# Optimization experiments

Measured on AMD Instinct MI355X. Metric: run time of the kernel, lower is better.

## Reference

```python
import jax, jax.numpy as jnp
import numpy as np

B, T, V, E, HID = 32, 128, 32000, 256, 512


def setup_inputs() -> dict:
    key = jax.random.key(0)
    ks = jax.random.split(key, 5)
    s_e, s_h, s_i, s_u = 1.0 / np.sqrt(E), 1.0 / np.sqrt(HID), 1.0 / np.sqrt(E), 1.0 / np.sqrt(HID)
    return {
        "input_x": jax.random.randint(ks[0], (B, T), 0, V, dtype=jnp.int32),
        "initial_state": jnp.zeros((B, HID), dtype=jnp.float32),
        "embedding": jax.random.normal(ks[1], (V, E), dtype=jnp.float32) * s_e,
        "H": jax.random.normal(ks[2], (HID, HID), dtype=jnp.float32) * s_h,
        "I": jax.random.normal(ks[3], (E, HID), dtype=jnp.float32) * s_i,
        "b1": jnp.zeros((HID,), dtype=jnp.float32),
        "U": jax.random.normal(ks[4], (HID, V), dtype=jnp.float32) * s_u,
        "b2": jnp.zeros((V,), dtype=jnp.float32),
    }


def reference(input_x, initial_state, embedding, H, I, b1, U, b2):
    # Embedding lookup: [B, T, E] -> time-major [T, B, E]
    emb = embedding[input_x]                      # [B, T, E]
    xs = jnp.transpose(emb, (1, 0, 2))            # [T, B, E]
    # Dropout is identity in eval mode (p=0.0).

    def step(h, x_t):
        h_new = jax.nn.relu(h @ H + x_t @ I + b1)  # [B, HID]
        return h_new, h_new

    last_state, hs = jax.lax.scan(step, initial_state, xs)  # hs: [T, B, HID]
    # Vocab projection for all steps at once: [T, B, V]
    logits = jnp.einsum("tbh,hv->tbv", hs, U) + b2
    logits = jnp.transpose(logits, (1, 0, 2))     # [B, T, V]
    return logits, last_state
```

## Files before the change

kernel.cpp:

```cpp
#include <hip/hip_runtime.h>
#include <hip/hip_bf16.h>
#include <stdint.h>

#define B_ 32
#define T_ 128
#define V_ 32000
#define E_ 256
#define HID_ 512

typedef float f32x4 __attribute__((ext_vector_type(4)));
typedef __bf16 bf16x8 __attribute__((ext_vector_type(8)));

static __device__ __forceinline__ unsigned short f2bf(float f) {
    unsigned int u = __float_as_uint(f);
    unsigned int r = (u + 0x7fffu + ((u >> 16) & 1u)) >> 16;
    return (unsigned short)r;
}

__global__ __launch_bounds__(512) void k_embed_proj(
    const int* __restrict__ x, const float* __restrict__ emb,
    const float* __restrict__ I, const float* __restrict__ b1,
    float* __restrict__ C) {
    __shared__ float e[16][E_];
    const int tid = threadIdx.x;
    const int row0 = blockIdx.x * 16;

#pragma unroll
    for (int p = 0; p < 2; ++p) {
        int flat = p * 2048 + tid * 4;
        int i = flat >> 8;
        int c = flat & 255;
        int r = row0 + i;
        int t = r >> 5, b = r & 31;
        int xi = x[b * T_ + t];
        *(f32x4*)&e[i][c] = *(const f32x4*)(emb + (size_t)xi * E_ + c);
    }
    __syncthreads();

    float acc[16];
#pragma unroll
    for (int i = 0; i < 16; ++i) acc[i] = 0.f;
    const int j = tid;

    for (int k4 = 0; k4 < E_ / 4; ++k4) {
        float Iv[4];
#pragma unroll
        for (int q = 0; q < 4; ++q) Iv[q] = I[(size_t)(k4 * 4 + q) * HID_ + j];
#pragma unroll
        for (int i = 0; i < 16; ++i) {
            f32x4 ev = *(const f32x4*)&e[i][k4 * 4];
            acc[i] += ev[0] * Iv[0];
            acc[i] += ev[1] * Iv[1];
            acc[i] += ev[2] * Iv[2];
            acc[i] += ev[3] * Iv[3];
        }
    }
    float bv = b1[j];
#pragma unroll
    for (int i = 0; i < 16; ++i)
        C[(size_t)(row0 + i) * HID_ + j] = acc[i] + bv;
}

__global__ __launch_bounds__(256) void k_hconv(const float* __restrict__ H,
                                               unsigned short* __restrict__ Hb) {
    int idx = (blockIdx.x * 256 + threadIdx.x) * 4;
    f32x4 v = *(const f32x4*)(H + idx);
    unsigned int p0 = (unsigned)f2bf(v[0]) | ((unsigned)f2bf(v[1]) << 16);
    unsigned int p1 = (unsigned)f2bf(v[2]) | ((unsigned)f2bf(v[3]) << 16);
    uint2 pp; pp.x = p0; pp.y = p1;
    *(uint2*)(Hb + idx) = pp;
}

__global__ __launch_bounds__(256) void k_transpose(const float* __restrict__ U,
                                                   unsigned short* __restrict__ Ut) {
    __shared__ float tile[64][65];
    const int tid = threadIdx.x;
    const int n0 = blockIdx.x * 64;
    const int k0 = blockIdx.y * 64;
    const int c = tid & 63;
    const int r = tid >> 6;
#pragma unroll
    for (int it = 0; it < 16; ++it) {
        int kk = it * 4 + r;
        tile[kk][c] = U[(size_t)(k0 + kk) * V_ + n0 + c];
    }
    __syncthreads();
#pragma unroll
    for (int it = 0; it < 16; ++it) {
        int nn = it * 4 + r;
        Ut[(size_t)(n0 + nn) * HID_ + k0 + c] = f2bf(tile[c][nn]);
    }
}

__global__ __launch_bounds__(512) void k_recur(
    const float* __restrict__ C, const unsigned short* __restrict__ Hb,
    const float* __restrict__ init, unsigned short* __restrict__ hsb,
    float* __restrict__ lastState) {
    __shared__ float h[HID_];
    __shared__ float ps[8][HID_];
    const int tid = threadIdx.x;
    const int b = blockIdx.x;
    const int kg = tid >> 6;
    const int cg = tid & 63;
    const int j0 = cg * 8;
    const int kbase = kg * 64;

    h[tid] = init[b * HID_ + tid];
    __syncthreads();

    for (int t = 0; t < T_; ++t) {
        float cv = C[((size_t)t * B_ + b) * HID_ + tid];
        float a0 = 0, a1 = 0, a2 = 0, a3 = 0, a4 = 0, a5 = 0, a6 = 0, a7 = 0;
#pragma unroll 4
        for (int k4 = 0; k4 < 16; ++k4) {
            f32x4 hv = *(const f32x4*)&h[kbase + k4 * 4];
#pragma unroll
            for (int q = 0; q < 4; ++q) {
                const uint4 u = *(const uint4*)(Hb + (size_t)(kbase + k4 * 4 + q) * HID_ + j0);
                float hq = hv[q];
                a0 += hq * __uint_as_float(u.x << 16);
                a1 += hq * __uint_as_float(u.x & 0xffff0000u);
                a2 += hq * __uint_as_float(u.y << 16);
                a3 += hq * __uint_as_float(u.y & 0xffff0000u);
                a4 += hq * __uint_as_float(u.z << 16);
                a5 += hq * __uint_as_float(u.z & 0xffff0000u);
                a6 += hq * __uint_as_float(u.w << 16);
                a7 += hq * __uint_as_float(u.w & 0xffff0000u);
            }
        }
        f32x4 w0 = {a0, a1, a2, a3};
        f32x4 w1 = {a4, a5, a6, a7};
        *(f32x4*)&ps[kg][j0] = w0;
        *(f32x4*)&ps[kg][j0 + 4] = w1;
        __syncthreads();

        float v = cv;
#pragma unroll
        for (int g = 0; g < 8; ++g) v += ps[g][tid];
        v = fmaxf(v, 0.f);
        h[tid] = v;
        hsb[((size_t)t * B_ + b) * HID_ + tid] = f2bf(v);
        __syncthreads();
    }
    lastState[b * HID_ + tid] = h[tid];
}

#define LDK 72
__global__ __launch_bounds__(256) void k_gemm(
    const unsigned short* __restrict__ A, const unsigned short* __restrict__ Bt,
    const float* __restrict__ b2, float* __restrict__ out) {
    __shared__ unsigned short As[128 * LDK];
    __shared__ unsigned short Bs[128 * LDK];
    const int tid = threadIdx.x;
    const int l = tid & 63;
    const int w = tid >> 6;
    const int wm = w >> 1, wn = w & 1;
    const int n0 = blockIdx.x * 128;
    const int m0 = blockIdx.y * 128;

    f32x4 acc[4][4] = {};

    for (int kt = 0; kt < 8; ++kt) {
        const int kk = kt * 64;
        uint4 ra[4], rb[4];
#pragma unroll
        for (int i = 0; i < 4; ++i) {
            int flat = i * 256 + tid;
            int row = flat >> 3;
            int c8 = (flat & 7) * 8;
            ra[i] = *(const uint4*)(A + (size_t)(m0 + row) * HID_ + kk + c8);
            rb[i] = *(const uint4*)(Bt + (size_t)(n0 + row) * HID_ + kk + c8);
        }
        __syncthreads();
#pragma unroll
        for (int i = 0; i < 4; ++i) {
            int flat = i * 256 + tid;
            int row = flat >> 3;
            int c8 = (flat & 7) * 8;
            *(uint4*)(As + row * LDK + c8) = ra[i];
            *(uint4*)(Bs + row * LDK + c8) = rb[i];
        }
        __syncthreads();
#pragma unroll
        for (int ks = 0; ks < 2; ++ks) {
            bf16x8 af[4], bfr[4];
#pragma unroll
            for (int f = 0; f < 4; ++f) {
                af[f]  = *(const bf16x8*)(As + (wm * 64 + f * 16 + (l & 15)) * LDK + ks * 32 + (l >> 4) * 8);
                bfr[f] = *(const bf16x8*)(Bs + (wn * 64 + f * 16 + (l & 15)) * LDK + ks * 32 + (l >> 4) * 8);
            }
#pragma unroll
            for (int fm = 0; fm < 4; ++fm)
#pragma unroll
                for (int fn = 0; fn < 4; ++fn)
                    acc[fm][fn] = __builtin_amdgcn_mfma_f32_16x16x32_bf16(
                        af[fm], bfr[fn], acc[fm][fn], 0, 0, 0);
        }
    }

    const int cl = l & 15;
    const int q4 = (l >> 4) * 4;
    float b2v[4];
#pragma unroll
    for (int fn = 0; fn < 4; ++fn) b2v[fn] = b2[n0 + wn * 64 + fn * 16 + cl];
#pragma unroll
    for (int fm = 0; fm < 4; ++fm) {
#pragma unroll
        for (int r = 0; r < 4; ++r) {
            int rg = m0 + wm * 64 + fm * 16 + q4 + r;
            int t = rg >> 5, b = rg & 31;
            float* orow = out + (size_t)(b * T_ + t) * V_ + n0 + wn * 64 + cl;
#pragma unroll
            for (int fn = 0; fn < 4; ++fn)
                orow[fn * 16] = acc[fm][fn][r] + b2v[fn];
        }
    }
}

extern "C" void kernel_launch(void* const* d_in, const int* in_sizes, int n_in,
                              void* d_out, int out_size, void* d_ws, size_t ws_size,
                              hipStream_t stream) {
    const int* x      = (const int*)d_in[0];
    const float* init = (const float*)d_in[1];
    const float* emb  = (const float*)d_in[2];
    const float* H    = (const float*)d_in[3];
    const float* I    = (const float*)d_in[4];
    const float* b1   = (const float*)d_in[5];
    const float* U    = (const float*)d_in[6];
    const float* b2   = (const float*)d_in[7];
    float* out = (float*)d_out;

    char* ws = (char*)d_ws;
    float* C            = (float*)ws;
    unsigned short* hsb = (unsigned short*)(ws + ((size_t)8 << 20));
    unsigned short* Ut  = (unsigned short*)(ws + ((size_t)12 << 20));
    unsigned short* Hb  = (unsigned short*)(ws + ((size_t)46 << 20));

    k_embed_proj<<<256, 512, 0, stream>>>(x, emb, I, b1, C);
    k_hconv<<<(HID_ * HID_) / (256 * 4), 256, 0, stream>>>(H, Hb);
    k_transpose<<<dim3(500, 8), 256, 0, stream>>>(U, Ut);
    k_recur<<<B_, 512, 0, stream>>>(C, Hb, init, hsb, out + (size_t)B_ * T_ * V_);
    k_gemm<<<dim3(250, 32), 256, 0, stream>>>(hsb, Ut, b2, out);
}
```

Measured before the change: 1.774 ms.

## Split recurrence across four blocks per batch with register-resident H slices

The recurrent kernel now uses four cooperating blocks per batch row, each holding a 128-row slice of the bf16 H matrix in registers instead of re-reading H from global memory every step. Partial sums are exchanged through a global scratch area (the output buffer, which the later GEMM overwrites) with per-step release/acquire flags, and the kernel is launched cooperatively with 128 blocks. This is meant to cut the per-step global-memory traffic for H and spread the serial recurrence over more CUs. In exchange it adds a cross-block flag handshake on every timestep, a memset, and pressure from 64 registers per thread for the H slice.

Measured after the change: 3.280 ms. 1.85x slower.

```diff
diff --git a/kernel.cpp b/kernel.cpp
--- a/kernel.cpp
+++ b/kernel.cpp
@@ -95,54 +95,88 @@
 __global__ __launch_bounds__(512) void k_recur(
     const float* __restrict__ C, const unsigned short* __restrict__ Hb,
     const float* __restrict__ init, unsigned short* __restrict__ hsb,
-    float* __restrict__ lastState) {
+    float* __restrict__ lastState, float* __restrict__ xbuf,
+    int* __restrict__ xflag) {
     __shared__ float h[HID_];
-    __shared__ float ps[8][HID_];
-    const int tid = threadIdx.x;
-    const int b = blockIdx.x;
-    const int kg = tid >> 6;
-    const int cg = tid & 63;
-    const int j0 = cg * 8;
-    const int kbase = kg * 64;
-
-    h[tid] = init[b * HID_ + tid];
+    __shared__ unsigned short stage[32][HID_];
+    const int tid = threadIdx.x;
+    const int b = blockIdx.x >> 2;
+    const int g = blockIdx.x & 3;
+    const int j = tid;
+
+    unsigned int Hreg[64];
+#pragma unroll
+    for (int c4 = 0; c4 < 4; ++c4) {
+#pragma unroll
+        for (int i = 0; i < 4; ++i) {
+            int idx = i * 512 + tid;
+            int rr = idx >> 6;
+            int col = (idx & 63) * 8;
+            *(uint4*)&stage[rr][col] =
+                *(const uint4*)(Hb + (size_t)(g * 128 + c4 * 32 + rr) * HID_ + col);
+        }
+        __syncthreads();
+#pragma unroll
+        for (int rr = 0; rr < 32; rr += 2) {
+            unsigned int lo = stage[rr][j];
+            unsigned int hi = stage[rr + 1][j];
+            Hreg[(c4 * 32 + rr) >> 1] = lo | (hi << 16);
+        }
+        __syncthreads();
+    }
+
+    if (tid < HID_) h[tid] = init[b * HID_ + tid];
     __syncthreads();
 
     for (int t = 0; t < T_; ++t) {
-        float cv = C[((size_t)t * B_ + b) * HID_ + tid];
-        float a0 = 0, a1 = 0, a2 = 0, a3 = 0, a4 = 0, a5 = 0, a6 = 0, a7 = 0;
-#pragma unroll 4
-        for (int k4 = 0; k4 < 16; ++k4) {
-            f32x4 hv = *(const f32x4*)&h[kbase + k4 * 4];
-#pragma unroll
-            for (int q = 0; q < 4; ++q) {
-                const uint4 u = *(const uint4*)(Hb + (size_t)(kbase + k4 * 4 + q) * HID_ + j0);
-                float hq = hv[q];
-                a0 += hq * __uint_as_float(u.x << 16);
-                a1 += hq * __uint_as_float(u.x & 0xffff0000u);
-                a2 += hq * __uint_as_float(u.y << 16);
-                a3 += hq * __uint_as_float(u.y & 0xffff0000u);
-                a4 += hq * __uint_as_float(u.z << 16);
-                a5 += hq * __uint_as_float(u.z & 0xffff0000u);
-                a6 += hq * __uint_as_float(u.w << 16);
-                a7 += hq * __uint_as_float(u.w & 0xffff0000u);
+        float cv = C[((size_t)t * B_ + b) * HID_ + j];
+        float acc = 0.f;
+#pragma unroll
+        for (int kb = 0; kb < 8; ++kb) {
+            f32x4 hv[4];
+#pragma unroll
+            for (int q = 0; q < 4; ++q)
+                hv[q] = *(const f32x4*)&h[g * 128 + kb * 16 + q * 4];
+#pragma unroll
+            for (int p = 0; p < 8; ++p) {
+                unsigned int u = Hreg[kb * 8 + p];
+                float hlo = hv[p >> 1][(2 * p) & 3];
+                float hhi = hv[p >> 1][(2 * p + 1) & 3];
+                acc += __uint_as_float(u << 16) * hlo;
+                acc += __uint_as_float(u & 0xffff0000u) * hhi;
             }
         }
-        f32x4 w0 = {a0, a1, a2, a3};
-        f32x4 w1 = {a4, a5, a6, a7};
-        *(f32x4*)&ps[kg][j0] = w0;
-        *(f32x4*)&ps[kg][j0 + 4] = w1;
+
+        const size_t base = ((size_t)t * B_ + b) * 4;
+        __hip_atomic_store(&xbuf[(base + g) * HID_ + j], acc,
+                           __ATOMIC_RELAXED, __HIP_MEMORY_SCOPE_AGENT);
+        __threadfence();
+        __syncthreads();
+        if (tid == 0)
+            __hip_atomic_store(&xflag[base + g], 1,
+                               __ATOMIC_RELEASE, __HIP_MEMORY_SCOPE_AGENT);
+        if (tid < 4 && tid != g) {
+            while (__hip_atomic_load(&xflag[base + tid],
+                                     __ATOMIC_ACQUIRE, __HIP_MEMORY_SCOPE_AGENT) == 0) {}
+        }
         __syncthreads();
 
         float v = cv;
 #pragma unroll
-        for (int g = 0; g < 8; ++g) v += ps[g][tid];
+        for (int gg = 0; gg < 4; ++gg) {
+            float pg = (gg == g) ? acc
+                     : __hip_atomic_load(&xbuf[(base + gg) * HID_ + j],
+                                         __ATOMIC_RELAXED, __HIP_MEMORY_SCOPE_AGENT);
+            v += pg;
+        }
         v = fmaxf(v, 0.f);
-        h[tid] = v;
-        hsb[((size_t)t * B_ + b) * HID_ + tid] = f2bf(v);
-        __syncthreads();
-    }
-    lastState[b * HID_ + tid] = h[tid];
+        __syncthreads();
+        h[j] = v;
+        if (g == 0)
+            hsb[((size_t)t * B_ + b) * HID_ + j] = f2bf(v);
+        __syncthreads();
+    }
+    if (g == 0) lastState[b * HID_ + j] = h[j];
 }
 
 #define LDK 72
@@ -235,10 +269,19 @@
     unsigned short* hsb = (unsigned short*)(ws + ((size_t)8 << 20));
     unsigned short* Ut  = (unsigned short*)(ws + ((size_t)12 << 20));
     unsigned short* Hb  = (unsigned short*)(ws + ((size_t)46 << 20));
-
+    int* xflag          = (int*)(ws + ((size_t)47 << 20));
+    float* xbuf = out;
+    float* lastState = out + (size_t)B_ * T_ * V_;
+
+    hipMemsetAsync(xflag, 0, (size_t)T_ * B_ * 4 * sizeof(int), stream);
     k_embed_proj<<<256, 512, 0, stream>>>(x, emb, I, b1, C);
     k_hconv<<<(HID_ * HID_) / (256 * 4), 256, 0, stream>>>(H, Hb);
     k_transpose<<<dim3(500, 8), 256, 0, stream>>>(U, Ut);
-    k_recur<<<B_, 512, 0, stream>>>(C, Hb, init, hsb, out + (size_t)B_ * T_ * V_);
+
+    void* kargs[] = {(void*)&C, (void*)&Hb, (void*)&init, (void*)&hsb,
+                     (void*)&lastState, (void*)&xbuf, (void*)&xflag};
+    hipLaunchCooperativeKernel((void*)k_recur, dim3(128), dim3(512),
+                               kargs, 0, stream);
+
     k_gemm<<<dim3(250, 32), 256, 0, stream>>>(hsb, Ut, b2, out);
 }
```

## Keep bf16 H resident in registers and LDS inside the recurrence kernel

Applied to the files above, without the earlier changes.

Repacks H into pairs of bf16 rows interleaved per column, then has each recurrent thread own one output column. The thread holds 384 rows of its column in 192 registers and reads the other 128 rows from a 128KB LDS array. This removes the per-step global or L2 reads of H and the cross-warp partial-sum reduction, leaving one dot product per thread. The cost is very high register pressure (192 registers for H alone, which may spill despite launch_bounds(512,2)) and a large LDS footprint.

After: 2.528 ms. 1.42x slower.

```diff
diff --git a/kernel.cpp b/kernel.cpp
--- a/kernel.cpp
+++ b/kernel.cpp
@@ -61,14 +61,19 @@
         C[(size_t)(row0 + i) * HID_ + j] = acc[i] + bv;
 }
 
-__global__ __launch_bounds__(256) void k_hconv(const float* __restrict__ H,
-                                               unsigned short* __restrict__ Hb) {
-    int idx = (blockIdx.x * 256 + threadIdx.x) * 4;
-    f32x4 v = *(const f32x4*)(H + idx);
-    unsigned int p0 = (unsigned)f2bf(v[0]) | ((unsigned)f2bf(v[1]) << 16);
-    unsigned int p1 = (unsigned)f2bf(v[2]) | ((unsigned)f2bf(v[3]) << 16);
-    uint2 pp; pp.x = p0; pp.y = p1;
-    *(uint2*)(Hb + idx) = pp;
+__global__ __launch_bounds__(256) void k_hpack(const float* __restrict__ H,
+                                               unsigned int* __restrict__ Hp) {
+    int idx = blockIdx.x * 256 + threadIdx.x;
+    int i = idx >> 7;
+    int j4 = (idx & 127) * 4;
+    f32x4 lo = *(const f32x4*)(H + (size_t)(2 * i) * HID_ + j4);
+    f32x4 hi = *(const f32x4*)(H + (size_t)(2 * i + 1) * HID_ + j4);
+    uint4 o;
+    o.x = (unsigned)f2bf(lo[0]) | ((unsigned)f2bf(hi[0]) << 16);
+    o.y = (unsigned)f2bf(lo[1]) | ((unsigned)f2bf(hi[1]) << 16);
+    o.z = (unsigned)f2bf(lo[2]) | ((unsigned)f2bf(hi[2]) << 16);
+    o.w = (unsigned)f2bf(lo[3]) | ((unsigned)f2bf(hi[3]) << 16);
+    *(uint4*)(Hp + (size_t)i * HID_ + j4) = o;
 }
 
 __global__ __launch_bounds__(256) void k_transpose(const float* __restrict__ U,
@@ -92,52 +97,58 @@
     }
 }
 
-__global__ __launch_bounds__(512) void k_recur(
-    const float* __restrict__ C, const unsigned short* __restrict__ Hb,
+__global__ __launch_bounds__(512, 2) void k_recur(
+    const float* __restrict__ C, const unsigned int* __restrict__ Hp,
     const float* __restrict__ init, unsigned short* __restrict__ hsb,
     float* __restrict__ lastState) {
     __shared__ float h[HID_];
-    __shared__ float ps[8][HID_];
+    __shared__ unsigned int Hl[64][HID_];
     const int tid = threadIdx.x;
     const int b = blockIdx.x;
-    const int kg = tid >> 6;
-    const int cg = tid & 63;
-    const int j0 = cg * 8;
-    const int kbase = kg * 64;
+
+    unsigned int Hreg[192];
+#pragma unroll
+    for (int i = 0; i < 192; ++i)
+        Hreg[i] = Hp[(size_t)i * HID_ + tid];
+#pragma unroll
+    for (int p = 0; p < 64; ++p)
+        Hl[p][tid] = Hp[(size_t)(192 + p) * HID_ + tid];
 
     h[tid] = init[b * HID_ + tid];
     __syncthreads();
 
     for (int t = 0; t < T_; ++t) {
         float cv = C[((size_t)t * B_ + b) * HID_ + tid];
-        float a0 = 0, a1 = 0, a2 = 0, a3 = 0, a4 = 0, a5 = 0, a6 = 0, a7 = 0;
-#pragma unroll 4
-        for (int k4 = 0; k4 < 16; ++k4) {
-            f32x4 hv = *(const f32x4*)&h[kbase + k4 * 4];
-#pragma unroll
-            for (int q = 0; q < 4; ++q) {
-                const uint4 u = *(const uint4*)(Hb + (size_t)(kbase + k4 * 4 + q) * HID_ + j0);
-                float hq = hv[q];
-                a0 += hq * __uint_as_float(u.x << 16);
-                a1 += hq * __uint_as_float(u.x & 0xffff0000u);
-                a2 += hq * __uint_as_float(u.y << 16);
-                a3 += hq * __uint_as_float(u.y & 0xffff0000u);
-                a4 += hq * __uint_as_float(u.z << 16);
-                a5 += hq * __uint_as_float(u.z & 0xffff0000u);
-                a6 += hq * __uint_as_float(u.w << 16);
-                a7 += hq * __uint_as_float(u.w & 0xffff0000u);
-            }
-        }
-        f32x4 w0 = {a0, a1, a2, a3};
-        f32x4 w1 = {a4, a5, a6, a7};
-        *(f32x4*)&ps[kg][j0] = w0;
-        *(f32x4*)&ps[kg][j0 + 4] = w1;
-        __syncthreads();
-
-        float v = cv;
-#pragma unroll
-        for (int g = 0; g < 8; ++g) v += ps[g][tid];
-        v = fmaxf(v, 0.f);
+        float a0 = 0.f, a1 = 0.f, a2 = 0.f, a3 = 0.f;
+#pragma unroll
+        for (int q = 0; q < 48; ++q) {
+            f32x4 h0 = *(const f32x4*)&h[q * 8];
+            f32x4 h1 = *(const f32x4*)&h[q * 8 + 4];
+            unsigned int u0 = Hreg[q * 4 + 0];
+            unsigned int u1 = Hreg[q * 4 + 1];
+            unsigned int u2 = Hreg[q * 4 + 2];
+            unsigned int u3 = Hreg[q * 4 + 3];
+            a0 += __uint_as_float(u0 << 16) * h0[0];
+            a1 += __uint_as_float(u0 & 0xffff0000u) * h0[1];
+            a2 += __uint_as_float(u1 << 16) * h0[2];
+            a3 += __uint_as_float(u1 & 0xffff0000u) * h0[3];
+            a0 += __uint_as_float(u2 << 16) * h1[0];
+            a1 += __uint_as_float(u2 & 0xffff0000u) * h1[1];
+            a2 += __uint_as_float(u3 << 16) * h1[2];
+            a3 += __uint_as_float(u3 & 0xffff0000u) * h1[3];
+        }
+#pragma unroll
+        for (int p = 0; p < 64; p += 2) {
+            unsigned int u0 = Hl[p][tid];
+            unsigned int u1 = Hl[p + 1][tid];
+            f32x4 hp = *(const f32x4*)&h[384 + 2 * p];
+            a0 += __uint_as_float(u0 << 16) * hp[0];
+            a1 += __uint_as_float(u0 & 0xffff0000u) * hp[1];
+            a2 += __uint_as_float(u1 << 16) * hp[2];
+            a3 += __uint_as_float(u1 & 0xffff0000u) * hp[3];
+        }
+        float v = fmaxf(cv + ((a0 + a1) + (a2 + a3)), 0.f);
+        __syncthreads();
         h[tid] = v;
         hsb[((size_t)t * B_ + b) * HID_ + tid] = f2bf(v);
         __syncthreads();
@@ -234,11 +245,12 @@
     float* C            = (float*)ws;
     unsigned short* hsb = (unsigned short*)(ws + ((size_t)8 << 20));
     unsigned short* Ut  = (unsigned short*)(ws + ((size_t)12 << 20));
-    unsigned short* Hb  = (unsigned short*)(ws + ((size_t)46 << 20));
+    unsigned int* Hp    = (unsigned int*)(ws + ((size_t)46 << 20));
+    float* lastState = out + (size_t)B_ * T_ * V_;
 
     k_embed_proj<<<256, 512, 0, stream>>>(x, emb, I, b1, C);
-    k_hconv<<<(HID_ * HID_) / (256 * 4), 256, 0, stream>>>(H, Hb);
+    k_hpack<<<128, 256, 0, stream>>>(H, Hp);
     k_transpose<<<dim3(500, 8), 256, 0, stream>>>(U, Ut);
-    k_recur<<<B_, 512, 0, stream>>>(C, Hb, init, hsb, out + (size_t)B_ * T_ * V_);
+    k_recur<<<B_, 512, 0, stream>>>(C, Hp, init, hsb, lastState);
     k_gemm<<<dim3(250, 32), 256, 0, stream>>>(hsb, Ut, b2, out);
 }
```
